# Kernel optimization log

Hardware: AMD Instinct MI355X
Metric: run time of the kernel (lower is better)

Reference implementation:

```python
import jax, jax.numpy as jnp
import numpy as np

OUT_SIZE = 7      # roi_layer out_size
SAMPLE_NUM = 2    # roi_layer sample_num
STRIDES = (4, 8, 16, 32)
IMG = 1024.0


def _roi_align(feat_nchw, rois, out, scale, sn):
    """mmdet RoIAlign (aligned=False), vectorized over all rois.

    feat_nchw: [B, C, H, W]; rois: [N, 5] = (batch_idx, x1, y1, x2, y2).
    Returns [N, C, out, out].
    """
    feat = jnp.transpose(feat_nchw, (0, 2, 3, 1))  # [B, H, W, C]
    B, H, W, C = feat.shape
    N = rois.shape[0]
    b = rois[:, 0].astype(jnp.int32)
    x1 = rois[:, 1] * scale
    y1 = rois[:, 2] * scale
    x2 = rois[:, 3] * scale
    y2 = rois[:, 4] * scale
    roi_w = jnp.maximum(x2 - x1, 1.0)
    roi_h = jnp.maximum(y2 - y1, 1.0)
    # sample-point offsets within the roi, in bin units: [out*sn]
    grid = (jnp.arange(out, dtype=jnp.float32)[:, None]
            + (jnp.arange(sn, dtype=jnp.float32)[None, :] + 0.5) / sn).reshape(-1)
    ys = y1[:, None] + grid[None, :] * (roi_h / out)[:, None]  # [N, S]
    xs = x1[:, None] + grid[None, :] * (roi_w / out)[:, None]  # [N, S]

    def interp1(coord, size):
        valid = ((coord > -1.0) & (coord < size)).astype(coord.dtype)
        c = jnp.clip(coord, 0.0, size - 1.0)
        lo = jnp.floor(c).astype(jnp.int32)
        hi = jnp.minimum(lo + 1, size - 1)
        w_hi = c - lo.astype(coord.dtype)
        w_lo = 1.0 - w_hi
        # zero-out out-of-image samples via the weights
        return lo, hi, w_lo * valid, w_hi * valid

    y_lo, y_hi, wy_lo, wy_hi = interp1(ys, H)
    x_lo, x_hi, wx_lo, wx_hi = interp1(xs, W)

    def gather(yi, xi):
        # [N, S, S, C]
        return feat[b[:, None, None], yi[:, :, None], xi[:, None, :]]

    val = (gather(y_lo, x_lo) * (wy_lo[:, :, None] * wx_lo[:, None, :])[..., None]
           + gather(y_lo, x_hi) * (wy_lo[:, :, None] * wx_hi[:, None, :])[..., None]
           + gather(y_hi, x_lo) * (wy_hi[:, :, None] * wx_lo[:, None, :])[..., None]
           + gather(y_hi, x_hi) * (wy_hi[:, :, None] * wx_hi[:, None, :])[..., None])
    # average the sn x sn samples inside each bin
    val = val.reshape(N, out, sn, out, sn, C).mean(axis=(2, 4))  # [N, out, out, C]
    return jnp.transpose(val, (0, 3, 1, 2))  # [N, C, out, out]


def setup_inputs() -> dict:
    key = jax.random.key(0)
    ks = jax.random.split(key, 8)
    feats = {}
    for i, hw in enumerate([256, 128, 64, 32]):
        feats[f"feat{i}"] = jax.random.normal(ks[i], (1, 256, hw, hw), dtype=jnp.float32)
    N = 1000
    u = jax.random.uniform(ks[4], (N, 4), dtype=jnp.float32)
    x1 = u[:, 0] * (IMG - 64.0)
    y1 = u[:, 1] * (IMG - 64.0)
    w = 16.0 + u[:, 2] * 480.0
    h = 16.0 + u[:, 3] * 480.0
    x2 = jnp.minimum(x1 + w, IMG - 1.0)
    y2 = jnp.minimum(y1 + h, IMG - 1.0)
    bidx = jnp.zeros((N,), dtype=jnp.float32)
    rois = jnp.stack([bidx, x1, y1, x2, y2], axis=1)
    feats["rois"] = rois
    return feats


def reference(feat0, feat1, feat2, feat3, rois):
    feats = (feat0, feat1, feat2, feat3)
    # PASingleRoIExtractor multi-level path: RoIAlign every roi on every level,
    # then elementwise max across levels.
    out = _roi_align(feats[0], rois, OUT_SIZE, 1.0 / STRIDES[0], SAMPLE_NUM)
    for lvl in range(1, len(feats)):
        out = jnp.maximum(out, _roi_align(feats[lvl], rois, OUT_SIZE,
                                          1.0 / STRIDES[lvl], SAMPLE_NUM))
    return out
```

## Files before the change

kernel.cpp:

```cpp
#include <hip/hip_runtime.h>


#define NCH 256
#define NBIN 49

typedef _Float16 half2v __attribute__((ext_vector_type(2)));

#if defined(__has_builtin)
#if __has_builtin(__builtin_amdgcn_fdot2)
#define HAVE_FDOT2 1
#endif
#if __has_builtin(__builtin_amdgcn_cvt_pkrtz)
#define HAVE_PKRTZ 1
#endif
#endif

__device__ __constant__ int    d_H[4]      = {256, 128, 64, 32};
__device__ __constant__ float  d_scale[4]  = {0.25f, 0.125f, 0.0625f, 0.03125f};
__device__ __constant__ unsigned d_off4b[4] = {0u, 33554432u, 41943040u, 44040192u};
__device__ __constant__ size_t d_offu[4]   = {0, 16777216, 20971520, 22020096};
__device__ __constant__ int    d_P[4]      = {65536, 16384, 4096, 1024};
__device__ __constant__ int    d_t2s[4]    = {0, 2048, 2560, 2688};
__device__ __constant__ int    d_psh[4]    = {9, 7, 5, 3};

__device__ __forceinline__ int pack_h2(float a, float b) {
#ifdef HAVE_PKRTZ
    return __builtin_bit_cast(int, __builtin_amdgcn_cvt_pkrtz(a, b));
#else
    half2v h;
    h.x = (_Float16)a;
    h.y = (_Float16)b;
    return __builtin_bit_cast(int, h);
#endif
}
__device__ __forceinline__ half2v bc_h2(int x) { return __builtin_bit_cast(half2v, x); }
__device__ __forceinline__ half2v bc_h2u(unsigned x) { return __builtin_bit_cast(half2v, x); }

#ifdef HAVE_FDOT2
#define ACC2(uLLc, uLHc, w2, k0)                                                                       \
    acc[k0] = __builtin_amdgcn_fdot2(bc_h2u(__builtin_amdgcn_perm((uLHc), (uLLc), 0x05040100u)), (w2), \
                                     acc[k0], false);                                                  \
    acc[k0 + 1] = __builtin_amdgcn_fdot2(                                                              \
        bc_h2u(__builtin_amdgcn_perm((uLHc), (uLLc), 0x07060302u)), (w2), acc[k0 + 1], false)
#else
#define ACC2(uLLc, uLHc, w2, k0)                                       \
    do {                                                               \
        half2v a_ = bc_h2u(uLLc), b_ = bc_h2u(uLHc);                   \
        float w0_ = (float)(w2).x, w1_ = (float)(w2).y;                \
        acc[k0]     = fmaf((float)a_.x, w0_, acc[k0]);                 \
        acc[k0]     = fmaf((float)b_.x, w1_, acc[k0]);                 \
        acc[k0 + 1] = fmaf((float)a_.y, w0_, acc[k0 + 1]);             \
        acc[k0 + 1] = fmaf((float)b_.y, w1_, acc[k0 + 1]);             \
    } while (0)
#endif

__device__ __forceinline__ void math4(float* acc, const uint4* L, int4 ye, int4 xe) {
    half2v wx = bc_h2(xe.z);
    half2v wlo = bc_h2(ye.z) * wx;
    half2v whi = bc_h2(ye.w) * wx;
    ACC2(L[0].x, L[1].x, wlo, 0);
    ACC2(L[0].y, L[1].y, wlo, 2);
    ACC2(L[0].z, L[1].z, wlo, 4);
    ACC2(L[0].w, L[1].w, wlo, 6);
    ACC2(L[2].x, L[3].x, whi, 0);
    ACC2(L[2].y, L[3].y, whi, 2);
    ACC2(L[2].z, L[3].z, whi, 4);
    ACC2(L[2].w, L[3].w, whi, 6);
}

__device__ __forceinline__ uint4 ldws(const char* __restrict__ wsb, unsigned off) {
    return *(const uint4*)(wsb + off);
}

__device__ __forceinline__ void issue16(uint4* L, const char* __restrict__ wsb, unsigned base,
                                        int4 ye0, int4 ye1, int4 xe0, int4 xe1) {
    L[0]  = ldws(wsb, base + (unsigned)(ye0.x + xe0.x));
    L[1]  = ldws(wsb, base + (unsigned)(ye0.x + xe0.y));
    L[2]  = ldws(wsb, base + (unsigned)(ye0.y + xe0.x));
    L[3]  = ldws(wsb, base + (unsigned)(ye0.y + xe0.y));
    L[4]  = ldws(wsb, base + (unsigned)(ye0.x + xe1.x));
    L[5]  = ldws(wsb, base + (unsigned)(ye0.x + xe1.y));
    L[6]  = ldws(wsb, base + (unsigned)(ye0.y + xe1.x));
    L[7]  = ldws(wsb, base + (unsigned)(ye0.y + xe1.y));
    L[8]  = ldws(wsb, base + (unsigned)(ye1.x + xe0.x));
    L[9]  = ldws(wsb, base + (unsigned)(ye1.x + xe0.y));
    L[10] = ldws(wsb, base + (unsigned)(ye1.y + xe0.x));
    L[11] = ldws(wsb, base + (unsigned)(ye1.y + xe0.y));
    L[12] = ldws(wsb, base + (unsigned)(ye1.x + xe1.x));
    L[13] = ldws(wsb, base + (unsigned)(ye1.x + xe1.y));
    L[14] = ldws(wsb, base + (unsigned)(ye1.y + xe1.x));
    L[15] = ldws(wsb, base + (unsigned)(ye1.y + xe1.y));
}

__device__ __forceinline__ void math_stage(float* m, const uint4* L, int4 ye0, int4 ye1,
                                           int4 xe0, int4 xe1) {
    float acc[8];
#pragma unroll
    for (int k = 0; k < 8; ++k) acc[k] = 0.0f;
    math4(acc, &L[0], ye0, xe0);
    math4(acc, &L[4], ye0, xe1);
    math4(acc, &L[8], ye1, xe0);
    math4(acc, &L[12], ye1, xe1);
#pragma unroll
    for (int k = 0; k < 8; ++k) m[k] = fmaxf(m[k], acc[k] * 0.25f);
}

__global__ __launch_bounds__(256) void transpose_flat(
    const float* __restrict__ f0, const float* __restrict__ f1, const float* __restrict__ f2,
    const float* __restrict__ f3, unsigned short* __restrict__ out) {
    const int b = blockIdx.x;
    const int lvl = (b >= d_t2s[1]) + (b >= d_t2s[2]) + (b >= d_t2s[3]);
    const int rem = b - d_t2s[lvl];
    const int sh = d_psh[lvl];
    const int pb = rem & ((1 << sh) - 1);
    const int cgi = rem >> sh;
    const int P = d_P[lvl];
    const float* in = (lvl == 0) ? f0 : (lvl == 1) ? f1 : (lvl == 2) ? f2 : f3;

    const int tid = threadIdx.x;
    const int o8 = tid & 7;
    const int g = tid >> 3;
    const int p0 = pb * 128 + g * 4;
    const int c0 = cgi * 64 + o8 * 8;

    const float* src = in + (size_t)c0 * P + p0;
    float vv[32];
#pragma unroll
    for (int r = 0; r < 8; ++r)
        *(float4*)&vv[4 * r] = *(const float4*)(src + (size_t)r * P);

    unsigned short* o = out + d_offu[lvl] + (size_t)p0 * NCH + c0;
#pragma unroll
    for (int j = 0; j < 4; ++j) {
        uint4 d;
        d.x = (unsigned)pack_h2(vv[0 * 4 + j], vv[1 * 4 + j]);
        d.y = (unsigned)pack_h2(vv[2 * 4 + j], vv[3 * 4 + j]);
        d.z = (unsigned)pack_h2(vv[4 * 4 + j], vv[5 * 4 + j]);
        d.w = (unsigned)pack_h2(vv[6 * 4 + j], vv[7 * 4 + j]);
        *(uint4*)(o + (size_t)j * NCH) = d;
    }
}

__global__ __launch_bounds__(256, 2) void roi_main4b(const uint4* __restrict__ ws,
                                                     const float* __restrict__ rois,
                                                     float* __restrict__ out) {
    __shared__ float smem[64 * NBIN];
    __shared__ int4 tbl[4][2][14];

    const int n = blockIdx.x >> 2;
    const int quarter = blockIdx.x & 3;
    const int tid = threadIdx.x;
    const float* r = rois + (size_t)n * 5;

    if (tid < 112) {
        int lvl = tid / 28;
        int e = tid % 28;
        int axis = e / 14;
        int s = e % 14;
        int H = d_H[lvl];
        float sc = d_scale[lvl];
        float a = (axis ? r[1] : r[2]) * sc;
        float b2 = (axis ? r[3] : r[4]) * sc;
        float binsz = fmaxf(b2 - a, 1.0f) * (1.0f / 7.0f);
        float g = (float)(s >> 1) + 0.25f + 0.5f * (float)(s & 1);
        float coord = a + g * binsz;
        float valid = (coord > -1.0f && coord < (float)H) ? 1.0f : 0.0f;
        float c = fminf(fmaxf(coord, 0.0f), (float)H - 1.0f);
        int lo = (int)floorf(c);
        int hi = min(lo + 1, H - 1);
        float whi = (c - (float)lo) * valid;
        float wlo = (1.0f - (c - (float)lo)) * valid;
        int mult = axis ? 512 : H * 512;
        int4 t;
        t.x = lo * mult;
        t.y = hi * mult;
        if (axis) {
            t.z = pack_h2(wlo, whi);
            t.w = 0;
        } else {
            t.z = pack_h2(wlo, wlo);
            t.w = pack_h2(whi, whi);
        }
        tbl[lvl][axis][s] = t;
    }
    __syncthreads();

    const int p = tid & 7;
    const int h = tid >> 3;
    const int octet = quarter * 8 + p;
    const char* __restrict__ wsb = (const char*)ws;

    unsigned lvlbase[4];
#pragma unroll
    for (int l = 0; l < 4; ++l) lvlbase[l] = d_off4b[l] + (unsigned)octet * 16u;

#define RD_E(E, lvl)                     \
    E##y0 = tbl[lvl][0][2 * by];         \
    E##y1 = tbl[lvl][0][2 * by + 1];     \
    E##x0 = tbl[lvl][1][2 * bx];         \
    E##x1 = tbl[lvl][1][2 * bx + 1]
#define ISSUE(L, E, lvl) issue16(L, wsb, lvlbase[lvl], E##y0, E##y1, E##x0, E##x1)
#define MATH(L, E) math_stage(m, L, E##y0, E##y1, E##x0, E##x1)
#define FENCE() __builtin_amdgcn_sched_barrier(0)

#pragma unroll
    for (int pass = 0; pass < 2; ++pass) {
        const int b = h + pass * 32;
        if (b < NBIN) {
            int by = b / 7;
            int bx = b - by * 7;
            float m[8];
#pragma unroll
            for (int k = 0; k < 8; ++k) m[k] = -3.402823e38f;

            uint4 LA[16], LB[16];
            int4 Ay0, Ay1, Ax0, Ax1, By0, By1, Bx0, Bx1;

            RD_E(A, 0);
            ISSUE(LA, A, 0);
            RD_E(B, 1);
            ISSUE(LB, B, 1);
            FENCE();
            MATH(LA, A);
            FENCE();
            RD_E(A, 2);
            ISSUE(LA, A, 2);
            FENCE();
            MATH(LB, B);
            FENCE();
            RD_E(B, 3);
            ISSUE(LB, B, 3);
            FENCE();
            MATH(LA, A);
            FENCE();
            MATH(LB, B);

#pragma unroll
            for (int k = 0; k < 8; ++k) smem[(p * 8 + k) * NBIN + b] = m[k];
        }
    }
#undef RD_E
#undef ISSUE
#undef MATH
#undef FENCE
    __syncthreads();

    float4* o4 = (float4*)(out + (size_t)n * (NCH * NBIN) + (size_t)quarter * (64 * NBIN));
    const float4* s4 = (const float4*)smem;
    for (int i = tid; i < 64 * NBIN / 4; i += 256) o4[i] = s4[i];
}

__device__ __forceinline__ int4 make_entry_f(float coord, int size, int mult) {
    float valid = (coord > -1.0f && coord < (float)size) ? 1.0f : 0.0f;
    float c = fminf(fmaxf(coord, 0.0f), (float)size - 1.0f);
    int lo = (int)floorf(c);
    int hi = min(lo + 1, size - 1);
    float whi = (c - (float)lo) * valid;
    float wlo = (1.0f - (c - (float)lo)) * valid;
    int4 r;
    r.x = lo * mult;
    r.y = hi * mult;
    r.z = __float_as_int(wlo);
    r.w = __float_as_int(whi);
    return r;
}

__global__ __launch_bounds__(256) void roi_direct(
    const float* __restrict__ f0, const float* __restrict__ f1, const float* __restrict__ f2,
    const float* __restrict__ f3, const float* __restrict__ rois, float* __restrict__ out) {
    const int n = blockIdx.x;
    const int c = threadIdx.x;
    const float* feats[4] = {f0, f1, f2, f3};
    const float* r = rois + (size_t)n * 5;
    for (int b = 0; b < NBIN; ++b) {
        int by = b / 7;
        int bx = b - by * 7;
        float m = -3.402823e38f;
#pragma unroll
        for (int lvl = 0; lvl < 4; ++lvl) {
            int H = d_H[lvl];
            float sc = d_scale[lvl];
            float x1 = r[1] * sc, y1 = r[2] * sc, x2 = r[3] * sc, y2 = r[4] * sc;
            float bw = fmaxf(x2 - x1, 1.0f) * (1.0f / 7.0f);
            float bh = fmaxf(y2 - y1, 1.0f) * (1.0f / 7.0f);
            const float* f = feats[lvl] + (size_t)c * H * H;
            float acc = 0.0f;
#pragma unroll
            for (int sy = 0; sy < 2; ++sy) {
#pragma unroll
                for (int sx = 0; sx < 2; ++sx) {
                    float yc = y1 + ((float)by + 0.25f + 0.5f * sy) * bh;
                    float xc = x1 + ((float)bx + 0.25f + 0.5f * sx) * bw;
                    int4 ey = make_entry_f(yc, H, H);
                    int4 ex = make_entry_f(xc, H, 1);
                    float wyl = __int_as_float(ey.z), wyh = __int_as_float(ey.w);
                    float wxl = __int_as_float(ex.z), wxh = __int_as_float(ex.w);
                    acc += f[ey.x + ex.x] * wyl * wxl + f[ey.x + ex.y] * wyl * wxh +
                           f[ey.y + ex.x] * wyh * wxl + f[ey.y + ex.y] * wyh * wxh;
                }
            }
            m = fmaxf(m, acc * 0.25f);
        }
        out[((size_t)n * NCH + c) * NBIN + b] = m;
    }
}

extern "C" void kernel_launch(void* const* d_in, const int* in_sizes, int n_in, void* d_out,
                              int out_size, void* d_ws, size_t ws_size, hipStream_t stream) {
    const float* f0 = (const float*)d_in[0];
    const float* f1 = (const float*)d_in[1];
    const float* f2 = (const float*)d_in[2];
    const float* f3 = (const float*)d_in[3];
    const float* rois = (const float*)d_in[4];
    const int nrois = in_sizes[4] / 5;
    float* out = (float*)d_out;

    const size_t need = 44564480;
    if (ws_size < need) {
        roi_direct<<<nrois, 256, 0, stream>>>(f0, f1, f2, f3, rois, out);
        return;
    }
    unsigned short* wsp = (unsigned short*)d_ws;
    transpose_flat<<<2720, 256, 0, stream>>>(f0, f1, f2, f3, wsp);
    roi_main4b<<<4 * nrois, 256, 0, stream>>>((const uint4*)d_ws, rois, out);
}
```

Before: 203.9 us.

## Split RoI work into single-wave blocks with XCD-aware remapping and direct stores

```diff
diff --git a/kernel.cpp b/kernel.cpp
--- a/kernel.cpp
+++ b/kernel.cpp
@@ -105,6 +105,39 @@
     for (int k = 0; k < 8; ++k) m[k] = fmaxf(m[k], acc[k] * 0.25f);
 }
 
+__device__ __forceinline__ void build_entry(int4 (*tbl)[2][14], const float* __restrict__ r,
+                                            int e) {
+    int lvl = e / 28;
+    int e2 = e % 28;
+    int axis = e2 / 14;
+    int s = e2 % 14;
+    int H = d_H[lvl];
+    float sc = d_scale[lvl];
+    float a = (axis ? r[1] : r[2]) * sc;
+    float b2 = (axis ? r[3] : r[4]) * sc;
+    float binsz = fmaxf(b2 - a, 1.0f) * (1.0f / 7.0f);
+    float g = (float)(s >> 1) + 0.25f + 0.5f * (float)(s & 1);
+    float coord = a + g * binsz;
+    float valid = (coord > -1.0f && coord < (float)H) ? 1.0f : 0.0f;
+    float c = fminf(fmaxf(coord, 0.0f), (float)H - 1.0f);
+    int lo = (int)floorf(c);
+    int hi = min(lo + 1, H - 1);
+    float whi = (c - (float)lo) * valid;
+    float wlo = (1.0f - (c - (float)lo)) * valid;
+    int mult = axis ? 512 : H * 512;
+    int4 t;
+    t.x = lo * mult;
+    t.y = hi * mult;
+    if (axis) {
+        t.z = pack_h2(wlo, whi);
+        t.w = 0;
+    } else {
+        t.z = pack_h2(wlo, wlo);
+        t.w = pack_h2(whi, whi);
+    }
+    tbl[lvl][axis][s] = t;
+}
+
 __global__ __launch_bounds__(256) void transpose_flat(
     const float* __restrict__ f0, const float* __restrict__ f1, const float* __restrict__ f2,
     const float* __restrict__ f3, unsigned short* __restrict__ out) {
@@ -141,52 +174,33 @@
     }
 }
 
-__global__ __launch_bounds__(256, 2) void roi_main4b(const uint4* __restrict__ ws,
-                                                     const float* __restrict__ rois,
-                                                     float* __restrict__ out) {
-    __shared__ float smem[64 * NBIN];
+__global__ __launch_bounds__(64, 4) void roi_main1w(const uint4* __restrict__ ws,
+                                                    const float* __restrict__ rois,
+                                                    float* __restrict__ out) {
     __shared__ int4 tbl[4][2][14];
 
-    const int n = blockIdx.x >> 2;
-    const int quarter = blockIdx.x & 3;
+    const int nwg = (int)gridDim.x;
+    const int orig = blockIdx.x;
+    const int xcd = orig & 7;
+    const int idx = orig >> 3;
+    const int q8 = nwg >> 3, r8 = nwg & 7;
+    const int wg = (xcd < r8 ? xcd * (q8 + 1) : r8 * (q8 + 1) + (xcd - r8) * q8) + idx;
+
+    const int n = wg / 28;
+    const int rem = wg - n * 28;
+    const int quarter = rem / 7;
+    const int bg = rem - quarter * 7;
+
     const int tid = threadIdx.x;
     const float* r = rois + (size_t)n * 5;
 
-    if (tid < 112) {
-        int lvl = tid / 28;
-        int e = tid % 28;
-        int axis = e / 14;
-        int s = e % 14;
-        int H = d_H[lvl];
-        float sc = d_scale[lvl];
-        float a = (axis ? r[1] : r[2]) * sc;
-        float b2 = (axis ? r[3] : r[4]) * sc;
-        float binsz = fmaxf(b2 - a, 1.0f) * (1.0f / 7.0f);
-        float g = (float)(s >> 1) + 0.25f + 0.5f * (float)(s & 1);
-        float coord = a + g * binsz;
-        float valid = (coord > -1.0f && coord < (float)H) ? 1.0f : 0.0f;
-        float c = fminf(fmaxf(coord, 0.0f), (float)H - 1.0f);
-        int lo = (int)floorf(c);
-        int hi = min(lo + 1, H - 1);
-        float whi = (c - (float)lo) * valid;
-        float wlo = (1.0f - (c - (float)lo)) * valid;
-        int mult = axis ? 512 : H * 512;
-        int4 t;
-        t.x = lo * mult;
-        t.y = hi * mult;
-        if (axis) {
-            t.z = pack_h2(wlo, whi);
-            t.w = 0;
-        } else {
-            t.z = pack_h2(wlo, wlo);
-            t.w = pack_h2(whi, whi);
-        }
-        tbl[lvl][axis][s] = t;
-    }
+    build_entry(tbl, r, tid);
+    if (tid < 112 - 64) build_entry(tbl, r, tid + 64);
     __syncthreads();
 
     const int p = tid & 7;
     const int h = tid >> 3;
+    const int b = bg * 8 + h;
     const int octet = quarter * 8 + p;
     const char* __restrict__ wsb = (const char*)ws;
 
@@ -203,51 +217,43 @@
 #define MATH(L, E) math_stage(m, L, E##y0, E##y1, E##x0, E##x1)
 #define FENCE() __builtin_amdgcn_sched_barrier(0)
 
-#pragma unroll
-    for (int pass = 0; pass < 2; ++pass) {
-        const int b = h + pass * 32;
-        if (b < NBIN) {
-            int by = b / 7;
-            int bx = b - by * 7;
-            float m[8];
-#pragma unroll
-            for (int k = 0; k < 8; ++k) m[k] = -3.402823e38f;
-
-            uint4 LA[16], LB[16];
-            int4 Ay0, Ay1, Ax0, Ax1, By0, By1, Bx0, Bx1;
-
-            RD_E(A, 0);
-            ISSUE(LA, A, 0);
-            RD_E(B, 1);
-            ISSUE(LB, B, 1);
-            FENCE();
-            MATH(LA, A);
-            FENCE();
-            RD_E(A, 2);
-            ISSUE(LA, A, 2);
-            FENCE();
-            MATH(LB, B);
-            FENCE();
-            RD_E(B, 3);
-            ISSUE(LB, B, 3);
-            FENCE();
-            MATH(LA, A);
-            FENCE();
-            MATH(LB, B);
-
-#pragma unroll
-            for (int k = 0; k < 8; ++k) smem[(p * 8 + k) * NBIN + b] = m[k];
-        }
+    if (b < NBIN) {
+        int by = b / 7;
+        int bx = b - by * 7;
+        float m[8];
+#pragma unroll
+        for (int k = 0; k < 8; ++k) m[k] = -3.402823e38f;
+
+        uint4 LA[16], LB[16];
+        int4 Ay0, Ay1, Ax0, Ax1, By0, By1, Bx0, Bx1;
+
+        RD_E(A, 0);
+        ISSUE(LA, A, 0);
+        RD_E(B, 1);
+        ISSUE(LB, B, 1);
+        FENCE();
+        MATH(LA, A);
+        FENCE();
+        RD_E(A, 2);
+        ISSUE(LA, A, 2);
+        FENCE();
+        MATH(LB, B);
+        FENCE();
+        RD_E(B, 3);
+        ISSUE(LB, B, 3);
+        FENCE();
+        MATH(LA, A);
+        FENCE();
+        MATH(LB, B);
+
+        float* o = out + (size_t)n * (NCH * NBIN) + (size_t)octet * 8 * NBIN + b;
+#pragma unroll
+        for (int k = 0; k < 8; ++k) o[(size_t)k * NBIN] = m[k];
     }
 #undef RD_E
 #undef ISSUE
 #undef MATH
 #undef FENCE
-    __syncthreads();
-
-    float4* o4 = (float4*)(out + (size_t)n * (NCH * NBIN) + (size_t)quarter * (64 * NBIN));
-    const float4* s4 = (const float4*)smem;
-    for (int i = tid; i < 64 * NBIN / 4; i += 256) o4[i] = s4[i];
 }
 
 __device__ __forceinline__ int4 make_entry_f(float coord, int size, int mult) {
@@ -322,5 +328,5 @@
     }
     unsigned short* wsp = (unsigned short*)d_ws;
     transpose_flat<<<2720, 256, 0, stream>>>(f0, f1, f2, f3, wsp);
-    roi_main4b<<<4 * nrois, 256, 0, stream>>>((const uint4*)d_ws, rois, out);
-}
+    roi_main1w<<<nrois * 28, 64, 0, stream>>>((const uint4*)d_ws, rois, out);
+}
```

Result: slower. 380.4 us (+86.6%).

## Sort RoIs by Morton tile and remap workgroups per XCD for L2 locality

Applied to the files above, without the earlier changes.

```diff
diff --git a/kernel.cpp b/kernel.cpp
--- a/kernel.cpp
+++ b/kernel.cpp
@@ -3,6 +3,7 @@
 
 #define NCH 256
 #define NBIN 49
+#define WS_F16_BYTES 44564480u
 
 typedef _Float16 half2v __attribute__((ext_vector_type(2)));
 
@@ -105,6 +106,49 @@
     for (int k = 0; k < 8; ++k) m[k] = fmaxf(m[k], acc[k] * 0.25f);
 }
 
+__global__ __launch_bounds__(256) void roi_sort(const float* __restrict__ rois, int nrois,
+                                                int* __restrict__ perm) {
+    __shared__ unsigned hist[256];
+    __shared__ unsigned offs[256];
+    const int tid = threadIdx.x;
+    hist[tid] = 0;
+    __syncthreads();
+    for (int i = tid; i < nrois; i += 256) {
+        const float* r = rois + (size_t)i * 5;
+        float cx = 0.5f * (r[1] + r[3]);
+        float cy = 0.5f * (r[2] + r[4]);
+        int tx = min(max((int)(cx * (1.0f / 64.0f)), 0), 15);
+        int ty = min(max((int)(cy * (1.0f / 64.0f)), 0), 15);
+        int k = 0;
+#pragma unroll
+        for (int bb = 0; bb < 4; ++bb)
+            k |= (((tx >> bb) & 1) << (2 * bb)) | (((ty >> bb) & 1) << (2 * bb + 1));
+        atomicAdd(&hist[k], 1u);
+    }
+    __syncthreads();
+    if (tid == 0) {
+        unsigned acc = 0;
+        for (int i = 0; i < 256; ++i) {
+            offs[i] = acc;
+            acc += hist[i];
+        }
+    }
+    __syncthreads();
+    for (int i = tid; i < nrois; i += 256) {
+        const float* r = rois + (size_t)i * 5;
+        float cx = 0.5f * (r[1] + r[3]);
+        float cy = 0.5f * (r[2] + r[4]);
+        int tx = min(max((int)(cx * (1.0f / 64.0f)), 0), 15);
+        int ty = min(max((int)(cy * (1.0f / 64.0f)), 0), 15);
+        int k = 0;
+#pragma unroll
+        for (int bb = 0; bb < 4; ++bb)
+            k |= (((tx >> bb) & 1) << (2 * bb)) | (((ty >> bb) & 1) << (2 * bb + 1));
+        unsigned pos = atomicAdd(&offs[k], 1u);
+        perm[pos] = i;
+    }
+}
+
 __global__ __launch_bounds__(256) void transpose_flat(
     const float* __restrict__ f0, const float* __restrict__ f1, const float* __restrict__ f2,
     const float* __restrict__ f3, unsigned short* __restrict__ out) {
@@ -143,12 +187,22 @@
 
 __global__ __launch_bounds__(256, 2) void roi_main4b(const uint4* __restrict__ ws,
                                                      const float* __restrict__ rois,
+                                                     const int* __restrict__ perm, int nrois,
                                                      float* __restrict__ out) {
     __shared__ float smem[64 * NBIN];
     __shared__ int4 tbl[4][2][14];
 
-    const int n = blockIdx.x >> 2;
-    const int quarter = blockIdx.x & 3;
+    const int nwg = (int)gridDim.x;
+    const int orig = blockIdx.x;
+    const int xcd = orig & 7;
+    const int idx = orig >> 3;
+    const int q8 = nwg >> 3, r8 = nwg & 7;
+    const int wg = (xcd < r8 ? xcd * (q8 + 1) : r8 * (q8 + 1) + (xcd - r8) * q8) + idx;
+
+    const int quarter = wg / nrois;
+    const int sidx = wg - quarter * nrois;
+    const int n = perm[sidx];
+
     const int tid = threadIdx.x;
     const float* r = rois + (size_t)n * 5;
 
@@ -315,12 +369,14 @@
     const int nrois = in_sizes[4] / 5;
     float* out = (float*)d_out;
 
-    const size_t need = 44564480;
+    const size_t need = (size_t)WS_F16_BYTES + (size_t)nrois * 4;
     if (ws_size < need) {
         roi_direct<<<nrois, 256, 0, stream>>>(f0, f1, f2, f3, rois, out);
         return;
     }
     unsigned short* wsp = (unsigned short*)d_ws;
+    int* perm = (int*)((char*)d_ws + WS_F16_BYTES);
+    roi_sort<<<1, 256, 0, stream>>>(rois, nrois, perm);
     transpose_flat<<<2720, 256, 0, stream>>>(f0, f1, f2, f3, wsp);
-    roi_main4b<<<4 * nrois, 256, 0, stream>>>((const uint4*)d_ws, rois, out);
-}
+    roi_main4b<<<4 * nrois, 256, 0, stream>>>((const uint4*)d_ws, rois, perm, nrois, out);
+}
```

Result: no change. 201.4 us (-1.2%).
